# Optimization experiments

Hardware: AMD Instinct MI355X
Metric: run time of the kernel (lower is better)

## Reference

```python
import jax, jax.numpy as jnp
import numpy as np

B, T, DIN, DOUT, RANK = 4, 1, 4096, 11008, 512


def setup_inputs() -> dict:
    key = jax.random.key(0)
    ks = jax.random.split(key, 7)
    inp = jax.random.normal(ks[0], (B, T, DIN), jnp.float32)
    weight = jax.random.normal(ks[1], (DOUT, DIN), jnp.float32) * (1.0 / np.sqrt(DIN))
    bias = jax.random.normal(ks[2], (DOUT,), jnp.float32) * 0.02
    U = jax.random.normal(ks[3], (DOUT, RANK), jnp.float32) * (1.0 / np.sqrt(RANK))
    S = jax.random.uniform(ks[4], (RANK,), jnp.float32, 0.1, 1.0)
    V = jax.random.normal(ks[5], (DIN, RANK), jnp.float32) * (1.0 / np.sqrt(DIN))
    scale = jax.random.uniform(ks[6], (DIN,), jnp.float32, 0.5, 1.5)
    threshold = jnp.full((1,), 0.674, jnp.float32)
    return {"input": inp, "weight": weight, "bias": bias, "U": U, "S": S,
            "V": V, "scale": scale, "threshold": threshold}


def reference(input, weight, bias, U, S, V, scale, threshold):
    # r_sparse mode, decoding path (num_tokens == 1)
    th = threshold[0]
    # mask from scaled magnitudes; piecewise-constant w.r.t. inputs
    s_mask = jax.lax.stop_gradient(
        (jnp.abs(input * scale[None, None, :]) > th).astype(input.dtype))
    # sparse GEMM on masked input: [B,T,DIN] x [DOUT,DIN]^T + bias
    sparse_out = jnp.einsum('btd,od->bto', input * s_mask, weight) + bias
    # low-rank compensation on the complement: x @ (V diag(S)) @ U^T
    lr = jnp.einsum('btd,dr->btr', input * (1.0 - s_mask), V * S[None, :])
    lr = jnp.einsum('btr,or->bto', lr, U)
    return sparse_out + lr
```

## Files before the change

### kernel.cpp

```cpp
#include <hip/hip_runtime.h>
#include <cmath>

constexpr int DIN  = 4096;
constexpr int DOUT = 11008;
constexpr int RANK = 512;
constexpr int NB   = 4;

constexpr int NCHUNK = 256;
constexpr int DCH    = DIN / NCHUNK;
constexpr int SPLITK = 2;

__global__ __launch_bounds__(512)
void lr_partial_kernel(const float* __restrict__ x,
                       const float* __restrict__ scale,
                       const float* __restrict__ thp,
                       const float* __restrict__ V,
                       float* __restrict__ partial,
                       float* __restrict__ xs)
{
    __shared__ float xc[NB * DCH];
    const int chunk = blockIdx.x;
    const int t = threadIdx.x;
    const float th = thp[0];
    if (t < NB * DCH) {
        const int b = t / DCH, dd = t % DCH;
        const int d = chunk * DCH + dd;
        const float xv = x[b * DIN + d];
        const bool keep = fabsf(xv * scale[d]) > th;
        xc[t] = keep ? 0.f : xv;
        xs[b * DIN + d] = keep ? xv : 0.f;
    }
    __syncthreads();
    const int r = t;
    float a0 = 0.f, a1 = 0.f, a2 = 0.f, a3 = 0.f;
    #pragma unroll
    for (int dd = 0; dd < DCH; ++dd) {
        const float v = V[(size_t)(chunk * DCH + dd) * RANK + r];
        a0 = fmaf(xc[0 * DCH + dd], v, a0);
        a1 = fmaf(xc[1 * DCH + dd], v, a1);
        a2 = fmaf(xc[2 * DCH + dd], v, a2);
        a3 = fmaf(xc[3 * DCH + dd], v, a3);
    }
    float* p = partial + (size_t)chunk * (NB * RANK) + r;
    p[0 * RANK] = a0;
    p[1 * RANK] = a1;
    p[2 * RANK] = a2;
    p[3 * RANK] = a3;
}

__global__ __launch_bounds__(256)
void lr_reduce_kernel(const float* __restrict__ partial,
                      const float* __restrict__ S,
                      float* __restrict__ lr)
{
    const int t = blockIdx.x * 256 + threadIdx.x;
    const int idx = t >> 4;
    const int s = t & 15;
    float sum = 0.f;
    #pragma unroll
    for (int j = 0; j < 16; ++j)
        sum += partial[(size_t)(s * 16 + j) * (NB * RANK) + idx];
    #pragma unroll
    for (int m = 8; m >= 1; m >>= 1)
        sum += __shfl_xor(sum, m, 64);
    if (s == 0)
        lr[idx] = sum * S[idx & (RANK - 1)];
}

__global__ __launch_bounds__(256)
void rsparse_main_kernel(const float* __restrict__ xs,
                         const float* __restrict__ W,
                         const float* __restrict__ U,
                         const float* __restrict__ lr,
                         float* __restrict__ part)
{
    const int tid  = threadIdx.x;
    const int wave = tid >> 6, lane = tid & 63;
    const int pair = blockIdx.x * 2 + (wave >> 1);
    const int kh   = wave & 1;
    const int o0 = pair * 2, o1 = o0 + 1;
    const int kbase = kh * (DIN / SPLITK / 4);

    const float4* __restrict__ W0 = (const float4*)(W + (size_t)o0 * DIN);
    const float4* __restrict__ W1 = (const float4*)(W + (size_t)o1 * DIN);
    const float4* __restrict__ XS = (const float4*)xs;

    float acc0[NB] = {0.f, 0.f, 0.f, 0.f};
    float acc1[NB] = {0.f, 0.f, 0.f, 0.f};

    #pragma unroll 4
    for (int k = 0; k < 8; ++k) {
        const int c = kbase + (k << 6) + lane;
        const float4 w0 = W0[c];
        const float4 w1 = W1[c];
        #pragma unroll
        for (int b = 0; b < NB; ++b) {
            const float4 xv = XS[b * 1024 + c];
            acc0[b] = fmaf(w0.x, xv.x, acc0[b]);
            acc0[b] = fmaf(w0.y, xv.y, acc0[b]);
            acc0[b] = fmaf(w0.z, xv.z, acc0[b]);
            acc0[b] = fmaf(w0.w, xv.w, acc0[b]);
            acc1[b] = fmaf(w1.x, xv.x, acc1[b]);
            acc1[b] = fmaf(w1.y, xv.y, acc1[b]);
            acc1[b] = fmaf(w1.z, xv.z, acc1[b]);
            acc1[b] = fmaf(w1.w, xv.w, acc1[b]);
        }
    }

    if (kh == 0) {
        const float4* __restrict__ U0 = (const float4*)(U + (size_t)o0 * RANK);
        const float4* __restrict__ U1 = (const float4*)(U + (size_t)o1 * RANK);
        const float4* __restrict__ LR = (const float4*)lr;
        #pragma unroll
        for (int j = 0; j < 2; ++j) {
            const int c = (j << 6) + lane;
            const float4 u0 = U0[c];
            const float4 u1 = U1[c];
            #pragma unroll
            for (int b = 0; b < NB; ++b) {
                const float4 lv = LR[b * 128 + c];
                acc0[b] = fmaf(u0.x, lv.x, acc0[b]);
                acc0[b] = fmaf(u0.y, lv.y, acc0[b]);
                acc0[b] = fmaf(u0.z, lv.z, acc0[b]);
                acc0[b] = fmaf(u0.w, lv.w, acc0[b]);
                acc1[b] = fmaf(u1.x, lv.x, acc1[b]);
                acc1[b] = fmaf(u1.y, lv.y, acc1[b]);
                acc1[b] = fmaf(u1.z, lv.z, acc1[b]);
                acc1[b] = fmaf(u1.w, lv.w, acc1[b]);
            }
        }
    }

    #pragma unroll
    for (int b = 0; b < NB; ++b) {
        #pragma unroll
        for (int m = 32; m >= 1; m >>= 1) {
            acc0[b] += __shfl_xor(acc0[b], m, 64);
            acc1[b] += __shfl_xor(acc1[b], m, 64);
        }
    }

    if (lane == 0) {
        float* p = part + (size_t)kh * (NB * DOUT);
        #pragma unroll
        for (int b = 0; b < NB; ++b) {
            p[b * DOUT + o0] = acc0[b];
            p[b * DOUT + o1] = acc1[b];
        }
    }
}

__global__ __launch_bounds__(256)
void final_add_kernel(const float* __restrict__ part,
                      const float* __restrict__ bias,
                      float* __restrict__ out)
{
    const int i = blockIdx.x * 256 + threadIdx.x;
    const int o = i % DOUT;
    out[i] = part[i] + part[NB * DOUT + i] + bias[o];
}

extern "C" void kernel_launch(void* const* d_in, const int* in_sizes, int n_in,
                              void* d_out, int out_size, void* d_ws, size_t ws_size,
                              hipStream_t stream)
{
    const float* x     = (const float*)d_in[0];
    const float* W     = (const float*)d_in[1];
    const float* bias  = (const float*)d_in[2];
    const float* U     = (const float*)d_in[3];
    const float* S     = (const float*)d_in[4];
    const float* V     = (const float*)d_in[5];
    const float* scale = (const float*)d_in[6];
    const float* thp   = (const float*)d_in[7];
    float* out = (float*)d_out;

    float* partial = (float*)d_ws;
    float* lr      = partial + (size_t)NCHUNK * NB * RANK;
    float* xs      = lr + NB * RANK;
    float* part    = xs + NB * DIN;

    lr_partial_kernel<<<NCHUNK, 512, 0, stream>>>(x, scale, thp, V, partial, xs);
    lr_reduce_kernel<<<(NB * RANK * 16) / 256, 256, 0, stream>>>(partial, S, lr);
    rsparse_main_kernel<<<DOUT / 4, 256, 0, stream>>>(xs, W, U, lr, part);
    final_add_kernel<<<(NB * DOUT) / 256, 256, 0, stream>>>(part, bias, out);
}
```

Before: 52.72 us.

## Stage activations in LDS, compute four output rows per wave, vectorize final add

```diff
diff --git a/kernel.cpp b/kernel.cpp
--- a/kernel.cpp
+++ b/kernel.cpp
@@ -9,6 +9,7 @@
 constexpr int NCHUNK = 256;
 constexpr int DCH    = DIN / NCHUNK;
 constexpr int SPLITK = 2;
+constexpr int KHALF4 = DIN / SPLITK / 4;
 
 __global__ __launch_bounds__(512)
 void lr_partial_kernel(const float* __restrict__ x,
@@ -74,79 +75,108 @@
                          const float* __restrict__ lr,
                          float* __restrict__ part)
 {
-    const int tid  = threadIdx.x;
+    __shared__ float4 sx4[NB * KHALF4];
+    const int tid = threadIdx.x;
+    const int kh  = blockIdx.y;
+
+    const float4* __restrict__ XSg = (const float4*)xs;
+    #pragma unroll
+    for (int i = tid; i < NB * KHALF4; i += 256) {
+        const int b = i >> 9, j4 = i & (KHALF4 - 1);
+        sx4[i] = XSg[b * (DIN / 4) + kh * KHALF4 + j4];
+    }
+    __syncthreads();
+
     const int wave = tid >> 6, lane = tid & 63;
-    const int pair = blockIdx.x * 2 + (wave >> 1);
-    const int kh   = wave & 1;
-    const int o0 = pair * 2, o1 = o0 + 1;
-    const int kbase = kh * (DIN / SPLITK / 4);
-
-    const float4* __restrict__ W0 = (const float4*)(W + (size_t)o0 * DIN);
-    const float4* __restrict__ W1 = (const float4*)(W + (size_t)o1 * DIN);
-    const float4* __restrict__ XS = (const float4*)xs;
-
-    float acc0[NB] = {0.f, 0.f, 0.f, 0.f};
-    float acc1[NB] = {0.f, 0.f, 0.f, 0.f};
-
-    #pragma unroll 4
+    const int o0 = (blockIdx.x * 4 + wave) * 4;
+
+    const float4* __restrict__ W0 = (const float4*)(W + (size_t)(o0 + 0) * DIN) + kh * KHALF4;
+    const float4* __restrict__ W1 = (const float4*)(W + (size_t)(o0 + 1) * DIN) + kh * KHALF4;
+    const float4* __restrict__ W2 = (const float4*)(W + (size_t)(o0 + 2) * DIN) + kh * KHALF4;
+    const float4* __restrict__ W3 = (const float4*)(W + (size_t)(o0 + 3) * DIN) + kh * KHALF4;
+
+    float acc[4][NB] = {};
+
+    #pragma unroll 2
     for (int k = 0; k < 8; ++k) {
-        const int c = kbase + (k << 6) + lane;
+        const int c = (k << 6) + lane;
         const float4 w0 = W0[c];
         const float4 w1 = W1[c];
+        const float4 w2 = W2[c];
+        const float4 w3 = W3[c];
         #pragma unroll
         for (int b = 0; b < NB; ++b) {
-            const float4 xv = XS[b * 1024 + c];
-            acc0[b] = fmaf(w0.x, xv.x, acc0[b]);
-            acc0[b] = fmaf(w0.y, xv.y, acc0[b]);
-            acc0[b] = fmaf(w0.z, xv.z, acc0[b]);
-            acc0[b] = fmaf(w0.w, xv.w, acc0[b]);
-            acc1[b] = fmaf(w1.x, xv.x, acc1[b]);
-            acc1[b] = fmaf(w1.y, xv.y, acc1[b]);
-            acc1[b] = fmaf(w1.z, xv.z, acc1[b]);
-            acc1[b] = fmaf(w1.w, xv.w, acc1[b]);
+            const float4 xv = sx4[b * KHALF4 + c];
+            acc[0][b] = fmaf(w0.x, xv.x, acc[0][b]);
+            acc[0][b] = fmaf(w0.y, xv.y, acc[0][b]);
+            acc[0][b] = fmaf(w0.z, xv.z, acc[0][b]);
+            acc[0][b] = fmaf(w0.w, xv.w, acc[0][b]);
+            acc[1][b] = fmaf(w1.x, xv.x, acc[1][b]);
+            acc[1][b] = fmaf(w1.y, xv.y, acc[1][b]);
+            acc[1][b] = fmaf(w1.z, xv.z, acc[1][b]);
+            acc[1][b] = fmaf(w1.w, xv.w, acc[1][b]);
+            acc[2][b] = fmaf(w2.x, xv.x, acc[2][b]);
+            acc[2][b] = fmaf(w2.y, xv.y, acc[2][b]);
+            acc[2][b] = fmaf(w2.z, xv.z, acc[2][b]);
+            acc[2][b] = fmaf(w2.w, xv.w, acc[2][b]);
+            acc[3][b] = fmaf(w3.x, xv.x, acc[3][b]);
+            acc[3][b] = fmaf(w3.y, xv.y, acc[3][b]);
+            acc[3][b] = fmaf(w3.z, xv.z, acc[3][b]);
+            acc[3][b] = fmaf(w3.w, xv.w, acc[3][b]);
         }
     }
 
     if (kh == 0) {
-        const float4* __restrict__ U0 = (const float4*)(U + (size_t)o0 * RANK);
-        const float4* __restrict__ U1 = (const float4*)(U + (size_t)o1 * RANK);
+        const float4* __restrict__ U0 = (const float4*)(U + (size_t)(o0 + 0) * RANK);
+        const float4* __restrict__ U1 = (const float4*)(U + (size_t)(o0 + 1) * RANK);
+        const float4* __restrict__ U2 = (const float4*)(U + (size_t)(o0 + 2) * RANK);
+        const float4* __restrict__ U3 = (const float4*)(U + (size_t)(o0 + 3) * RANK);
         const float4* __restrict__ LR = (const float4*)lr;
         #pragma unroll
         for (int j = 0; j < 2; ++j) {
             const int c = (j << 6) + lane;
             const float4 u0 = U0[c];
             const float4 u1 = U1[c];
+            const float4 u2 = U2[c];
+            const float4 u3 = U3[c];
             #pragma unroll
             for (int b = 0; b < NB; ++b) {
                 const float4 lv = LR[b * 128 + c];
-                acc0[b] = fmaf(u0.x, lv.x, acc0[b]);
-                acc0[b] = fmaf(u0.y, lv.y, acc0[b]);
-                acc0[b] = fmaf(u0.z, lv.z, acc0[b]);
-                acc0[b] = fmaf(u0.w, lv.w, acc0[b]);
-                acc1[b] = fmaf(u1.x, lv.x, acc1[b]);
-                acc1[b] = fmaf(u1.y, lv.y, acc1[b]);
-                acc1[b] = fmaf(u1.z, lv.z, acc1[b]);
-                acc1[b] = fmaf(u1.w, lv.w, acc1[b]);
+                acc[0][b] = fmaf(u0.x, lv.x, acc[0][b]);
+                acc[0][b] = fmaf(u0.y, lv.y, acc[0][b]);
+                acc[0][b] = fmaf(u0.z, lv.z, acc[0][b]);
+                acc[0][b] = fmaf(u0.w, lv.w, acc[0][b]);
+                acc[1][b] = fmaf(u1.x, lv.x, acc[1][b]);
+                acc[1][b] = fmaf(u1.y, lv.y, acc[1][b]);
+                acc[1][b] = fmaf(u1.z, lv.z, acc[1][b]);
+                acc[1][b] = fmaf(u1.w, lv.w, acc[1][b]);
+                acc[2][b] = fmaf(u2.x, lv.x, acc[2][b]);
+                acc[2][b] = fmaf(u2.y, lv.y, acc[2][b]);
+                acc[2][b] = fmaf(u2.z, lv.z, acc[2][b]);
+                acc[2][b] = fmaf(u2.w, lv.w, acc[2][b]);
+                acc[3][b] = fmaf(u3.x, lv.x, acc[3][b]);
+                acc[3][b] = fmaf(u3.y, lv.y, acc[3][b]);
+                acc[3][b] = fmaf(u3.z, lv.z, acc[3][b]);
+                acc[3][b] = fmaf(u3.w, lv.w, acc[3][b]);
             }
         }
     }
 
     #pragma unroll
-    for (int b = 0; b < NB; ++b) {
-        #pragma unroll
-        for (int m = 32; m >= 1; m >>= 1) {
-            acc0[b] += __shfl_xor(acc0[b], m, 64);
-            acc1[b] += __shfl_xor(acc1[b], m, 64);
-        }
-    }
+    for (int r = 0; r < 4; ++r)
+        #pragma unroll
+        for (int b = 0; b < NB; ++b)
+            #pragma unroll
+            for (int m = 32; m >= 1; m >>= 1)
+                acc[r][b] += __shfl_xor(acc[r][b], m, 64);
 
     if (lane == 0) {
         float* p = part + (size_t)kh * (NB * DOUT);
         #pragma unroll
-        for (int b = 0; b < NB; ++b) {
-            p[b * DOUT + o0] = acc0[b];
-            p[b * DOUT + o1] = acc1[b];
-        }
+        for (int r = 0; r < 4; ++r)
+            #pragma unroll
+            for (int b = 0; b < NB; ++b)
+                p[b * DOUT + o0 + r] = acc[r][b];
     }
 }
 
@@ -155,9 +185,17 @@
                       const float* __restrict__ bias,
                       float* __restrict__ out)
 {
-    const int i = blockIdx.x * 256 + threadIdx.x;
-    const int o = i % DOUT;
-    out[i] = part[i] + part[NB * DOUT + i] + bias[o];
+    const int i4 = blockIdx.x * 256 + threadIdx.x;
+    const int o4 = i4 % (DOUT / 4);
+    const float4 p0 = ((const float4*)part)[i4];
+    const float4 p1 = ((const float4*)part)[NB * DOUT / 4 + i4];
+    const float4 bv = ((const float4*)bias)[o4];
+    float4 r;
+    r.x = p0.x + p1.x + bv.x;
+    r.y = p0.y + p1.y + bv.y;
+    r.z = p0.z + p1.z + bv.z;
+    r.w = p0.w + p1.w + bv.w;
+    ((float4*)out)[i4] = r;
 }
 
 extern "C" void kernel_launch(void* const* d_in, const int* in_sizes, int n_in,
@@ -181,6 +219,8 @@
 
     lr_partial_kernel<<<NCHUNK, 512, 0, stream>>>(x, scale, thp, V, partial, xs);
     lr_reduce_kernel<<<(NB * RANK * 16) / 256, 256, 0, stream>>>(partial, S, lr);
-    rsparse_main_kernel<<<DOUT / 4, 256, 0, stream>>>(xs, W, U, lr, part);
-    final_add_kernel<<<(NB * DOUT) / 256, 256, 0, stream>>>(part, bias, out);
-}
+
+    dim3 grid(DOUT / 16, SPLITK);
+    rsparse_main_kernel<<<grid, 256, 0, stream>>>(xs, W, U, lr, part);
+    final_add_kernel<<<(NB * DOUT / 4) / 256, 256, 0, stream>>>(part, bias, out);
+}
```

After: 57.60 us. +9.3%, slower.

## Split main GEMV K into sixteen slices with four rows per wave

Applied to the files above, without the earlier changes.

```diff
diff --git a/kernel.cpp b/kernel.cpp
--- a/kernel.cpp
+++ b/kernel.cpp
@@ -8,7 +8,11 @@
 
 constexpr int NCHUNK = 256;
 constexpr int DCH    = DIN / NCHUNK;
-constexpr int SPLITK = 2;
+
+constexpr int NSL = 16;
+constexpr int SL4 = 64;
+constexpr int RPW = 4;
+constexpr int ROWS_PER_BLOCK = 4 * RPW;
 
 __global__ __launch_bounds__(512)
 void lr_partial_kernel(const float* __restrict__ x,
@@ -76,77 +80,71 @@
 {
     const int tid  = threadIdx.x;
     const int wave = tid >> 6, lane = tid & 63;
-    const int pair = blockIdx.x * 2 + (wave >> 1);
-    const int kh   = wave & 1;
-    const int o0 = pair * 2, o1 = o0 + 1;
-    const int kbase = kh * (DIN / SPLITK / 4);
-
-    const float4* __restrict__ W0 = (const float4*)(W + (size_t)o0 * DIN);
-    const float4* __restrict__ W1 = (const float4*)(W + (size_t)o1 * DIN);
-    const float4* __restrict__ XS = (const float4*)xs;
-
-    float acc0[NB] = {0.f, 0.f, 0.f, 0.f};
-    float acc1[NB] = {0.f, 0.f, 0.f, 0.f};
-
-    #pragma unroll 4
-    for (int k = 0; k < 8; ++k) {
-        const int c = kbase + (k << 6) + lane;
-        const float4 w0 = W0[c];
-        const float4 w1 = W1[c];
+    const int s  = blockIdx.y;
+    const int o0 = blockIdx.x * ROWS_PER_BLOCK + wave * RPW;
+    const int c  = s * SL4 + lane;
+
+    const float4* __restrict__ XSg = (const float4*)xs;
+    float4 xr[NB];
+    #pragma unroll
+    for (int b = 0; b < NB; ++b)
+        xr[b] = XSg[b * (DIN / 4) + c];
+
+    float4 w[RPW];
+    #pragma unroll
+    for (int r = 0; r < RPW; ++r)
+        w[r] = ((const float4*)(W + (size_t)(o0 + r) * DIN))[c];
+
+    float acc[RPW][NB] = {};
+    #pragma unroll
+    for (int r = 0; r < RPW; ++r) {
         #pragma unroll
         for (int b = 0; b < NB; ++b) {
-            const float4 xv = XS[b * 1024 + c];
-            acc0[b] = fmaf(w0.x, xv.x, acc0[b]);
-            acc0[b] = fmaf(w0.y, xv.y, acc0[b]);
-            acc0[b] = fmaf(w0.z, xv.z, acc0[b]);
-            acc0[b] = fmaf(w0.w, xv.w, acc0[b]);
-            acc1[b] = fmaf(w1.x, xv.x, acc1[b]);
-            acc1[b] = fmaf(w1.y, xv.y, acc1[b]);
-            acc1[b] = fmaf(w1.z, xv.z, acc1[b]);
-            acc1[b] = fmaf(w1.w, xv.w, acc1[b]);
+            acc[r][b] = fmaf(w[r].x, xr[b].x, acc[r][b]);
+            acc[r][b] = fmaf(w[r].y, xr[b].y, acc[r][b]);
+            acc[r][b] = fmaf(w[r].z, xr[b].z, acc[r][b]);
+            acc[r][b] = fmaf(w[r].w, xr[b].w, acc[r][b]);
         }
     }
 
-    if (kh == 0) {
-        const float4* __restrict__ U0 = (const float4*)(U + (size_t)o0 * RANK);
-        const float4* __restrict__ U1 = (const float4*)(U + (size_t)o1 * RANK);
+    if (s == 0) {
         const float4* __restrict__ LR = (const float4*)lr;
         #pragma unroll
-        for (int j = 0; j < 2; ++j) {
-            const int c = (j << 6) + lane;
-            const float4 u0 = U0[c];
-            const float4 u1 = U1[c];
+        for (int r = 0; r < RPW; ++r) {
+            const float4* __restrict__ Ur = (const float4*)(U + (size_t)(o0 + r) * RANK);
+            const float4 u0 = Ur[lane];
+            const float4 u1 = Ur[64 + lane];
             #pragma unroll
             for (int b = 0; b < NB; ++b) {
-                const float4 lv = LR[b * 128 + c];
-                acc0[b] = fmaf(u0.x, lv.x, acc0[b]);
-                acc0[b] = fmaf(u0.y, lv.y, acc0[b]);
-                acc0[b] = fmaf(u0.z, lv.z, acc0[b]);
-                acc0[b] = fmaf(u0.w, lv.w, acc0[b]);
-                acc1[b] = fmaf(u1.x, lv.x, acc1[b]);
-                acc1[b] = fmaf(u1.y, lv.y, acc1[b]);
-                acc1[b] = fmaf(u1.z, lv.z, acc1[b]);
-                acc1[b] = fmaf(u1.w, lv.w, acc1[b]);
+                const float4 l0 = LR[b * 128 + lane];
+                const float4 l1 = LR[b * 128 + 64 + lane];
+                acc[r][b] = fmaf(u0.x, l0.x, acc[r][b]);
+                acc[r][b] = fmaf(u0.y, l0.y, acc[r][b]);
+                acc[r][b] = fmaf(u0.z, l0.z, acc[r][b]);
+                acc[r][b] = fmaf(u0.w, l0.w, acc[r][b]);
+                acc[r][b] = fmaf(u1.x, l1.x, acc[r][b]);
+                acc[r][b] = fmaf(u1.y, l1.y, acc[r][b]);
+                acc[r][b] = fmaf(u1.z, l1.z, acc[r][b]);
+                acc[r][b] = fmaf(u1.w, l1.w, acc[r][b]);
             }
         }
     }
 
     #pragma unroll
-    for (int b = 0; b < NB; ++b) {
-        #pragma unroll
-        for (int m = 32; m >= 1; m >>= 1) {
-            acc0[b] += __shfl_xor(acc0[b], m, 64);
-            acc1[b] += __shfl_xor(acc1[b], m, 64);
-        }
-    }
+    for (int r = 0; r < RPW; ++r)
+        #pragma unroll
+        for (int b = 0; b < NB; ++b)
+            #pragma unroll
+            for (int m = 32; m >= 1; m >>= 1)
+                acc[r][b] += __shfl_xor(acc[r][b], m, 64);
 
     if (lane == 0) {
-        float* p = part + (size_t)kh * (NB * DOUT);
-        #pragma unroll
-        for (int b = 0; b < NB; ++b) {
-            p[b * DOUT + o0] = acc0[b];
-            p[b * DOUT + o1] = acc1[b];
-        }
+        float* p = part + (size_t)s * (NB * DOUT);
+        #pragma unroll
+        for (int r = 0; r < RPW; ++r)
+            #pragma unroll
+            for (int b = 0; b < NB; ++b)
+                p[b * DOUT + o0 + r] = acc[r][b];
     }
 }
 
@@ -155,9 +153,35 @@
                       const float* __restrict__ bias,
                       float* __restrict__ out)
 {
-    const int i = blockIdx.x * 256 + threadIdx.x;
-    const int o = i % DOUT;
-    out[i] = part[i] + part[NB * DOUT + i] + bias[o];
+    const int t  = blockIdx.x * 256 + threadIdx.x;
+    const int i4 = t >> 2;
+    const int q  = t & 3;
+    const float4* p4 = (const float4*)part;
+    const int stride4 = NB * DOUT / 4;
+
+    float4 sum = {0.f, 0.f, 0.f, 0.f};
+    #pragma unroll
+    for (int j = 0; j < 4; ++j) {
+        const float4 v = p4[(size_t)(q * 4 + j) * stride4 + i4];
+        sum.x += v.x; sum.y += v.y; sum.z += v.z; sum.w += v.w;
+    }
+    #pragma unroll
+    for (int m = 1; m <= 2; m <<= 1) {
+        sum.x += __shfl_xor(sum.x, m, 64);
+        sum.y += __shfl_xor(sum.y, m, 64);
+        sum.z += __shfl_xor(sum.z, m, 64);
+        sum.w += __shfl_xor(sum.w, m, 64);
+    }
+    if (q == 0) {
+        const int o4 = i4 % (DOUT / 4);
+        const float4 bv = ((const float4*)bias)[o4];
+        float4 r;
+        r.x = sum.x + bv.x;
+        r.y = sum.y + bv.y;
+        r.z = sum.z + bv.z;
+        r.w = sum.w + bv.w;
+        ((float4*)out)[i4] = r;
+    }
 }
 
 extern "C" void kernel_launch(void* const* d_in, const int* in_sizes, int n_in,
@@ -181,6 +205,8 @@
 
     lr_partial_kernel<<<NCHUNK, 512, 0, stream>>>(x, scale, thp, V, partial, xs);
     lr_reduce_kernel<<<(NB * RANK * 16) / 256, 256, 0, stream>>>(partial, S, lr);
-    rsparse_main_kernel<<<DOUT / 4, 256, 0, stream>>>(xs, W, U, lr, part);
+
+    dim3 grid(DOUT / ROWS_PER_BLOCK, NSL);
+    rsparse_main_kernel<<<grid, 256, 0, stream>>>(xs, W, U, lr, part);
     final_add_kernel<<<(NB * DOUT) / 256, 256, 0, stream>>>(part, bias, out);
 }
```

New measurement: 68.47 us. +29.9%, slower.

## Switch main GEMV to thread-per-output-row with 32-way split-K slices

Applied to the files above, without the earlier changes.

```diff
diff --git a/kernel.cpp b/kernel.cpp
--- a/kernel.cpp
+++ b/kernel.cpp
@@ -8,7 +8,11 @@
 
 constexpr int NCHUNK = 256;
 constexpr int DCH    = DIN / NCHUNK;
-constexpr int SPLITK = 2;
+
+constexpr int NSL = 32;
+constexpr int SL4 = DIN / NSL / 4;
+constexpr int USL = 8;
+constexpr int UR4 = RANK / USL / 4;
 
 __global__ __launch_bounds__(512)
 void lr_partial_kernel(const float* __restrict__ x,
@@ -74,80 +78,48 @@
                          const float* __restrict__ lr,
                          float* __restrict__ part)
 {
-    const int tid  = threadIdx.x;
-    const int wave = tid >> 6, lane = tid & 63;
-    const int pair = blockIdx.x * 2 + (wave >> 1);
-    const int kh   = wave & 1;
-    const int o0 = pair * 2, o1 = o0 + 1;
-    const int kbase = kh * (DIN / SPLITK / 4);
+    const int o = blockIdx.x * 256 + threadIdx.x;
+    const int s = blockIdx.y;
 
-    const float4* __restrict__ W0 = (const float4*)(W + (size_t)o0 * DIN);
-    const float4* __restrict__ W1 = (const float4*)(W + (size_t)o1 * DIN);
-    const float4* __restrict__ XS = (const float4*)xs;
+    const float4* __restrict__ Wr = (const float4*)(W + (size_t)o * DIN) + s * SL4;
+    const float*  xsb = xs + s * (DIN / NSL);
 
-    float acc0[NB] = {0.f, 0.f, 0.f, 0.f};
-    float acc1[NB] = {0.f, 0.f, 0.f, 0.f};
+    float acc[NB] = {0.f, 0.f, 0.f, 0.f};
 
-    #pragma unroll 4
-    for (int k = 0; k < 8; ++k) {
-        const int c = kbase + (k << 6) + lane;
-        const float4 w0 = W0[c];
-        const float4 w1 = W1[c];
+    #pragma unroll
+    for (int k = 0; k < SL4; ++k) {
+        const float4 w = Wr[k];
         #pragma unroll
         for (int b = 0; b < NB; ++b) {
-            const float4 xv = XS[b * 1024 + c];
-            acc0[b] = fmaf(w0.x, xv.x, acc0[b]);
-            acc0[b] = fmaf(w0.y, xv.y, acc0[b]);
-            acc0[b] = fmaf(w0.z, xv.z, acc0[b]);
-            acc0[b] = fmaf(w0.w, xv.w, acc0[b]);
-            acc1[b] = fmaf(w1.x, xv.x, acc1[b]);
-            acc1[b] = fmaf(w1.y, xv.y, acc1[b]);
-            acc1[b] = fmaf(w1.z, xv.z, acc1[b]);
-            acc1[b] = fmaf(w1.w, xv.w, acc1[b]);
+            const float4 xv = *(const float4*)(xsb + b * DIN + 4 * k);
+            acc[b] = fmaf(w.x, xv.x, acc[b]);
+            acc[b] = fmaf(w.y, xv.y, acc[b]);
+            acc[b] = fmaf(w.z, xv.z, acc[b]);
+            acc[b] = fmaf(w.w, xv.w, acc[b]);
         }
     }
 
-    if (kh == 0) {
-        const float4* __restrict__ U0 = (const float4*)(U + (size_t)o0 * RANK);
-        const float4* __restrict__ U1 = (const float4*)(U + (size_t)o1 * RANK);
-        const float4* __restrict__ LR = (const float4*)lr;
+    if (s < USL) {
+        const float4* __restrict__ Ur = (const float4*)(U + (size_t)o * RANK) + s * UR4;
+        const float* lrb = lr + s * (RANK / USL);
         #pragma unroll
-        for (int j = 0; j < 2; ++j) {
-            const int c = (j << 6) + lane;
-            const float4 u0 = U0[c];
-            const float4 u1 = U1[c];
+        for (int k = 0; k < UR4; ++k) {
+            const float4 u = Ur[k];
             #pragma unroll
             for (int b = 0; b < NB; ++b) {
-                const float4 lv = LR[b * 128 + c];
-                acc0[b] = fmaf(u0.x, lv.x, acc0[b]);
-                acc0[b] = fmaf(u0.y, lv.y, acc0[b]);
-                acc0[b] = fmaf(u0.z, lv.z, acc0[b]);
-                acc0[b] = fmaf(u0.w, lv.w, acc0[b]);
-                acc1[b] = fmaf(u1.x, lv.x, acc1[b]);
-                acc1[b] = fmaf(u1.y, lv.y, acc1[b]);
-                acc1[b] = fmaf(u1.z, lv.z, acc1[b]);
-                acc1[b] = fmaf(u1.w, lv.w, acc1[b]);
+                const float4 lv = *(const float4*)(lrb + b * RANK + 4 * k);
+                acc[b] = fmaf(u.x, lv.x, acc[b]);
+                acc[b] = fmaf(u.y, lv.y, acc[b]);
+                acc[b] = fmaf(u.z, lv.z, acc[b]);
+                acc[b] = fmaf(u.w, lv.w, acc[b]);
             }
         }
     }
 
+    float* p = part + (size_t)s * (NB * DOUT) + o;
     #pragma unroll
-    for (int b = 0; b < NB; ++b) {
-        #pragma unroll
-        for (int m = 32; m >= 1; m >>= 1) {
-            acc0[b] += __shfl_xor(acc0[b], m, 64);
-            acc1[b] += __shfl_xor(acc1[b], m, 64);
-        }
-    }
-
-    if (lane == 0) {
-        float* p = part + (size_t)kh * (NB * DOUT);
-        #pragma unroll
-        for (int b = 0; b < NB; ++b) {
-            p[b * DOUT + o0] = acc0[b];
-            p[b * DOUT + o1] = acc1[b];
-        }
-    }
+    for (int b = 0; b < NB; ++b)
+        p[b * DOUT] = acc[b];
 }
 
 __global__ __launch_bounds__(256)
@@ -157,7 +129,11 @@
 {
     const int i = blockIdx.x * 256 + threadIdx.x;
     const int o = i % DOUT;
-    out[i] = part[i] + part[NB * DOUT + i] + bias[o];
+    float sum = 0.f;
+    #pragma unroll
+    for (int s = 0; s < NSL; ++s)
+        sum += part[(size_t)s * (NB * DOUT) + i];
+    out[i] = sum + bias[o];
 }
 
 extern "C" void kernel_launch(void* const* d_in, const int* in_sizes, int n_in,
@@ -181,6 +157,8 @@
 
     lr_partial_kernel<<<NCHUNK, 512, 0, stream>>>(x, scale, thp, V, partial, xs);
     lr_reduce_kernel<<<(NB * RANK * 16) / 256, 256, 0, stream>>>(partial, S, lr);
-    rsparse_main_kernel<<<DOUT / 4, 256, 0, stream>>>(xs, W, U, lr, part);
+
+    dim3 grid(DOUT / 256, NSL);
+    rsparse_main_kernel<<<grid, 256, 0, stream>>>(xs, W, U, lr, part);
     final_add_kernel<<<(NB * DOUT) / 256, 256, 0, stream>>>(part, bias, out);
 }
```

New measurement: 65.99 us. 25.2% more time.
